# Kernel optimization log

Hardware: AMD Instinct MI355X
Metric: run time of the kernel (lower is better)

Reference implementation:

```python
import jax, jax.numpy as jnp
import numpy as np

EPS = 1e-12  # matches torch F.normalize eps


def setup_inputs() -> dict:
    key = jax.random.key(0)
    k1, k2, k3 = jax.random.split(key, 3)
    N, C, H, W, K = 16, 1024, 32, 32, 32
    x = jax.random.normal(k1, (N, C, H, W), dtype=jnp.float32)
    # 1x1 conv weight (K, C, 1, 1) stored as (K, C)
    conv_w = jax.random.normal(k2, (K, C), dtype=jnp.float32) * 0.02
    centroids = jax.random.uniform(k3, (K, C), dtype=jnp.float32)
    return {"x": x, "conv_w": conv_w, "centroids": centroids}


def _l2norm(v, axis):
    return v / jnp.maximum(jnp.linalg.norm(v, axis=axis, keepdims=True), EPS)


def reference(x, conv_w, centroids):
    N, C, H, W = x.shape
    K = centroids.shape[0]
    # normalize_input: L2 over channel dim
    x = _l2norm(x, axis=1)
    xf = x.reshape(N, C, H * W)                      # (N, C, P)
    # 1x1 conv == per-pixel matmul -> (N, K, P)
    logits = jnp.einsum('kc,ncp->nkp', conv_w, xf)
    a = jax.nn.softmax(logits, axis=1)               # softmax over clusters
    # sum_p a[n,k,p] * (x[n,:,p] - centroids[k,:])
    # == (a @ x^T) - (sum_p a) * centroids  (two GEMMs, no (N,K,C,P) blowup)
    vlad = jnp.einsum('nkp,ncp->nkc', a, xf) - a.sum(-1)[:, :, None] * centroids[None]
    vlad = _l2norm(vlad, axis=2)                     # intra-cluster L2 norm
    vlad = vlad.reshape(N, K * C)
    vlad = _l2norm(vlad, axis=1)                     # global L2 norm
    return vlad
```

## Files before the change

### kernel.cpp

```cpp
#include <hip/hip_runtime.h>

#define NB   16
#define CC   1024
#define PP   1024
#define KK   32
#define EPSF 1e-12f

typedef __attribute__((ext_vector_type(8))) short  bf16x8;
typedef __attribute__((ext_vector_type(4))) float  f32x4;

__device__ __forceinline__ float bf2f(unsigned short u) {
    union { unsigned int i; float f; } v; v.i = ((unsigned int)u) << 16; return v.f;
}
__device__ __forceinline__ unsigned short f2bf(float f) {
    union { float f; unsigned int i; } v; v.f = f;
    return (unsigned short)((v.i + 0x7fffu + ((v.i >> 16) & 1u)) >> 16);
}

template <typename T> struct IO;
template <> struct IO<float> {
    static __device__ __forceinline__ float  ld (const float* p) { return *p; }
    static __device__ __forceinline__ float4 ld4(const float* p) { return *(const float4*)p; }
};
template <> struct IO<unsigned short> {
    static __device__ __forceinline__ float  ld (const unsigned short* p) { return bf2f(*p); }
    static __device__ __forceinline__ float4 ld4(const unsigned short* p) {
        const ushort4 u = *(const ushort4*)p;
        return make_float4(bf2f(u.x), bf2f(u.y), bf2f(u.z), bf2f(u.w));
    }
};

__device__ __forceinline__ void wg_sync_fast() {
    asm volatile("s_waitcnt lgkmcnt(0)" ::: "memory");
    __builtin_amdgcn_s_barrier();
    asm volatile("" ::: "memory");
}

__global__ __launch_bounds__(256) void k_detect(const unsigned short* __restrict__ xu,
                                                int* __restrict__ flag,
                                                float* __restrict__ zbuf) {
    __shared__ int s;
    const int t = threadIdx.x;
    for (int i = t; i < 2 * NB * KK; i += 256) zbuf[i] = 0.f;
    if (t == 0) s = 0;
    __syncthreads();
    int bad = 0;
    for (int i = t; i < 4096; i += 256)
        if (((xu[i] >> 7) & 0xFFu) > 0x9Fu) bad = 1;
    if (bad) atomicOr(&s, 1);
    __syncthreads();
    if (t == 0) flag[0] = s;
}

template <typename T>
__device__ __forceinline__ void attn_body(const T* __restrict__ x,
                                          const T* __restrict__ w,
                                          float* __restrict__ rnorm_ws,
                                          unsigned short* __restrict__ attn_g,
                                          float* __restrict__ asum) {
    __shared__ __align__(16) unsigned short xt[2][32 * 136];
    __shared__ __align__(16) unsigned short w_lds[2][32 * 136];
    __shared__ float red[32 * 32];
    __shared__ float lg[32 * 33];
    __shared__ float inv_lds[32];
    __shared__ float rnorm_lds[32];
    const int b = blockIdx.x, t = threadIdx.x;
    const int n = b >> 5, pbase = (b & 31) * 32;
    const int lane = t & 63, wid = t >> 6;
    const int quad = lane >> 4, l15 = lane & 15;
    const int mt = wid & 1, nt = wid >> 1;

    const size_t xb = (size_t)n * CC * PP + pbase;
    float ss0 = 0.f, ss1 = 0.f, ss2 = 0.f, ss3 = 0.f;
    f32x4 acc = {0.f, 0.f, 0.f, 0.f};

    const int pxg = 4 * (t & 7);
    const int crow = t >> 3;
    const int wcg = (t & 7) * 16;

    float4 xr[4], wr[4];
    #pragma unroll
    for (int pass = 0; pass < 4; ++pass)
        xr[pass] = IO<T>::ld4(&x[xb + (size_t)(crow + 32 * pass) * PP + pxg]);
    #pragma unroll
    for (int j = 0; j < 4; ++j)
        wr[j] = IO<T>::ld4(&w[crow * CC + wcg + 4 * j]);

    #pragma unroll 2
    for (int ch = 0; ch < 8; ++ch) {
        const int buf = ch & 1;
        #pragma unroll
        for (int pass = 0; pass < 4; ++pass) {
            const int cl = crow + 32 * pass;
            const float4 v = xr[pass];
            ss0 += v.x * v.x; ss1 += v.y * v.y; ss2 += v.z * v.z; ss3 += v.w * v.w;
            xt[buf][(pxg + 0) * 136 + cl] = f2bf(v.x);
            xt[buf][(pxg + 1) * 136 + cl] = f2bf(v.y);
            xt[buf][(pxg + 2) * 136 + cl] = f2bf(v.z);
            xt[buf][(pxg + 3) * 136 + cl] = f2bf(v.w);
        }
        #pragma unroll
        for (int j = 0; j < 4; ++j) {
            const float4 v = wr[j];
            ushort4 u;
            u.x = f2bf(v.x); u.y = f2bf(v.y); u.z = f2bf(v.z); u.w = f2bf(v.w);
            *(ushort4*)&w_lds[buf][crow * 136 + wcg + 4 * j] = u;
        }
        if (ch < 7) {
            const int c0 = (ch + 1) * 128;
            #pragma unroll
            for (int pass = 0; pass < 4; ++pass)
                xr[pass] = IO<T>::ld4(&x[xb + (size_t)(c0 + crow + 32 * pass) * PP + pxg]);
            #pragma unroll
            for (int j = 0; j < 4; ++j)
                wr[j] = IO<T>::ld4(&w[crow * CC + c0 + wcg + 4 * j]);
        }
        wg_sync_fast();
        #pragma unroll
        for (int ks = 0; ks < 4; ++ks) {
            const bf16x8 av = *(const bf16x8*)&xt[buf][(mt * 16 + l15) * 136 + ks * 32 + quad * 8];
            const bf16x8 bv = *(const bf16x8*)&w_lds[buf][(nt * 16 + l15) * 136 + ks * 32 + quad * 8];
            acc = __builtin_amdgcn_mfma_f32_16x16x32_bf16(av, bv, acc, 0, 0, 0);
        }
    }
    red[crow * 32 + pxg + 0] = ss0;
    red[crow * 32 + pxg + 1] = ss1;
    red[crow * 32 + pxg + 2] = ss2;
    red[crow * 32 + pxg + 3] = ss3;
    __syncthreads();
    if (t < 32) {
        float s = 0.f;
        #pragma unroll
        for (int g = 0; g < 32; ++g) s += red[g * 32 + t];
        const float r = 1.0f / fmaxf(sqrtf(s), EPSF);
        rnorm_lds[t] = r;
        rnorm_ws[n * PP + pbase + t] = r;
    }
    __syncthreads();
    #pragma unroll
    for (int reg = 0; reg < 4; ++reg) {
        const int px = mt * 16 + quad * 4 + reg;
        lg[px * 33 + nt * 16 + l15] = acc[reg] * rnorm_lds[px];
    }
    __syncthreads();
    if (t < 32) {
        float m = -1e30f;
        #pragma unroll
        for (int k = 0; k < KK; ++k) m = fmaxf(m, lg[t * 33 + k]);
        float s = 0.f;
        #pragma unroll
        for (int k = 0; k < KK; ++k) {
            const float e = expf(lg[t * 33 + k] - m);
            lg[t * 33 + k] = e;
            s += e;
        }
        inv_lds[t] = 1.0f / s;
    }
    __syncthreads();
    {
        const int k = t >> 3;
        float s = 0.f;
        ushort4 u;
        float vv[4];
        #pragma unroll
        for (int j = 0; j < 4; ++j) {
            const int px = pxg + j;
            vv[j] = lg[px * 33 + k] * inv_lds[px];
        }
        u.x = f2bf(vv[0]); u.y = f2bf(vv[1]); u.z = f2bf(vv[2]); u.w = f2bf(vv[3]);
        s = bf2f(u.x) + bf2f(u.y) + bf2f(u.z) + bf2f(u.w);
        *(ushort4*)&attn_g[((size_t)n * KK + k) * PP + pbase + pxg] = u;
        s += __shfl_xor(s, 1, 64);
        s += __shfl_xor(s, 2, 64);
        s += __shfl_xor(s, 4, 64);
        if ((t & 7) == 0) atomicAdd(&asum[n * KK + k], s);
    }
}
__global__ __launch_bounds__(256) void k_attn(const void* __restrict__ x,
                                              const void* __restrict__ w,
                                              const int* __restrict__ flag,
                                              float* __restrict__ rnorm_ws,
                                              unsigned short* __restrict__ attn_g,
                                              float* __restrict__ asum) {
    if (*flag) attn_body<float>((const float*)x, (const float*)w, rnorm_ws, attn_g, asum);
    else       attn_body<unsigned short>((const unsigned short*)x, (const unsigned short*)w,
                                         rnorm_ws, attn_g, asum);
}

template <typename T>
__device__ __forceinline__ void vlad_body(const T* __restrict__ x,
                                          const T* __restrict__ cent,
                                          const float* __restrict__ rnorm_ws,
                                          const unsigned short* __restrict__ attn_g,
                                          const float* __restrict__ asum,
                                          float* __restrict__ vlad,
                                          float* __restrict__ ssqnk) {
    __shared__ __align__(16) unsigned short xt[2][32 * 136];
    __shared__ __align__(16) unsigned short at_lds[2][32 * 136];
    __shared__ float asum_lds[32];
    __shared__ float ssq_lds[32];
    const int b = blockIdx.x, t = threadIdx.x;
    const int n = b >> 5, cbase = (b & 31) * 32;
    const int lane = t & 63, wid = t >> 6;
    const int quad = lane >> 4, l15 = lane & 15;
    const int mt = wid & 1, nt = wid >> 1;

    if (t < 32) { asum_lds[t] = asum[n * KK + t]; ssq_lds[t] = 0.f; }

    f32x4 acc = {0.f, 0.f, 0.f, 0.f};
    const size_t xb = (size_t)n * CC * PP + (size_t)cbase * PP;

    const int ak  = t >> 3, apg = (t & 7) * 16;
    const int xpg = 4 * (t & 31);
    const int xc  = t >> 5;

    uint4 a0, a1; float4 xr[4]; float4 rn;
    {
        const size_t abase = ((size_t)n * KK + ak) * PP + apg;
        a0 = *(const uint4*)&attn_g[abase];
        a1 = *(const uint4*)&attn_g[abase + 8];
        rn = *(const float4*)&rnorm_ws[n * PP + xpg];
        #pragma unroll
        for (int pass = 0; pass < 4; ++pass)
            xr[pass] = IO<T>::ld4(&x[xb + (size_t)(xc + 8 * pass) * PP + xpg]);
    }

    #pragma unroll 2
    for (int pc = 0; pc < 8; ++pc) {
        const int buf = pc & 1;
        *(uint4*)&at_lds[buf][ak * 136 + apg]     = a0;
        *(uint4*)&at_lds[buf][ak * 136 + apg + 8] = a1;
        #pragma unroll
        for (int pass = 0; pass < 4; ++pass) {
            const int ci = xc + 8 * pass;
            const float4 v = xr[pass];
            ushort4 u;
            u.x = f2bf(v.x * rn.x); u.y = f2bf(v.y * rn.y);
            u.z = f2bf(v.z * rn.z); u.w = f2bf(v.w * rn.w);
            *(ushort4*)&xt[buf][ci * 136 + xpg] = u;
        }
        if (pc < 7) {
            const int p0 = (pc + 1) * 128;
            const size_t abase = ((size_t)n * KK + ak) * PP + p0 + apg;
            a0 = *(const uint4*)&attn_g[abase];
            a1 = *(const uint4*)&attn_g[abase + 8];
            rn = *(const float4*)&rnorm_ws[n * PP + p0 + xpg];
            #pragma unroll
            for (int pass = 0; pass < 4; ++pass)
                xr[pass] = IO<T>::ld4(&x[xb + (size_t)(xc + 8 * pass) * PP + p0 + xpg]);
        }
        wg_sync_fast();
        #pragma unroll
        for (int ks = 0; ks < 4; ++ks) {
            const bf16x8 av = *(const bf16x8*)&at_lds[buf][(mt * 16 + l15) * 136 + ks * 32 + quad * 8];
            const bf16x8 bv = *(const bf16x8*)&xt[buf][(nt * 16 + l15) * 136 + ks * 32 + quad * 8];
            acc = __builtin_amdgcn_mfma_f32_16x16x32_bf16(av, bv, acc, 0, 0, 0);
        }
    }
    const int cg = cbase + nt * 16 + l15;
    #pragma unroll
    for (int reg = 0; reg < 4; ++reg) {
        const int k = mt * 16 + quad * 4 + reg;
        const float A = asum_lds[k];
        const float v0 = acc[reg] - A * IO<T>::ld(&cent[k * CC + cg]);
        vlad[((size_t)n * KK + k) * CC + cg] = v0;
        float s = v0 * v0;
        s += __shfl_xor(s, 1, 64);
        s += __shfl_xor(s, 2, 64);
        s += __shfl_xor(s, 4, 64);
        s += __shfl_xor(s, 8, 64);
        if (l15 == 0) atomicAdd(&ssq_lds[k], s);
    }
    __syncthreads();
    if (t < 32) atomicAdd(&ssqnk[n * KK + t], ssq_lds[t]);
}
__global__ __launch_bounds__(256) void k_vlad(const void* __restrict__ x,
                                              const void* __restrict__ cent,
                                              const int* __restrict__ flag,
                                              const float* __restrict__ rnorm_ws,
                                              const unsigned short* __restrict__ attn_g,
                                              const float* __restrict__ asum,
                                              float* __restrict__ vlad,
                                              float* __restrict__ ssqnk) {
    if (*flag) vlad_body<float>((const float*)x, (const float*)cent, rnorm_ws, attn_g,
                                asum, vlad, ssqnk);
    else       vlad_body<unsigned short>((const unsigned short*)x, (const unsigned short*)cent,
                                         rnorm_ws, attn_g, asum, vlad, ssqnk);
}

__global__ __launch_bounds__(256) void k_out(const float* __restrict__ vlad,
                                             const float* __restrict__ ssqnk,
                                             const int* __restrict__ flag,
                                             void* __restrict__ out) {
    __shared__ float fsh;
    const int b = blockIdx.x, t = threadIdx.x;
    const int n = b >> 5, k = b & 31;
    if (t < 64) {
        const float s = (t < 32) ? ssqnk[n * KK + t] : 0.f;
        const float r = 1.0f / fmaxf(sqrtf(s), EPSF);
        float g = s * r * r;
        #pragma unroll
        for (int off = 32; off > 0; off >>= 1) g += __shfl_down(g, off, 64);
        const float rk = __shfl(r, k, 64);
        if (t == 0) fsh = rk * (1.0f / fmaxf(sqrtf(g), EPSF));
    }
    __syncthreads();
    const float f = fsh;
    const float4 v = ((const float4*)(vlad + (size_t)b * CC))[t];
    if (*flag) {
        float4 o; o.x = v.x * f; o.y = v.y * f; o.z = v.z * f; o.w = v.w * f;
        ((float4*)((float*)out + (size_t)b * CC))[t] = o;
    } else {
        ushort4 u;
        u.x = f2bf(v.x * f); u.y = f2bf(v.y * f);
        u.z = f2bf(v.z * f); u.w = f2bf(v.w * f);
        ((ushort4*)((unsigned short*)out + (size_t)b * CC))[t] = u;
    }
}

extern "C" void kernel_launch(void* const* d_in, const int* in_sizes, int n_in,
                              void* d_out, int out_size, void* d_ws, size_t ws_size,
                              hipStream_t stream) {
    const void* x    = d_in[0];
    const void* w    = d_in[1];
    const void* cent = d_in[2];

    float* ws       = (float*)d_ws;
    float* rnorm_ws = ws;
    float* vlad     = rnorm_ws + NB * PP;
    float* asum     = vlad + NB * KK * CC;
    float* ssqnk    = asum + NB * KK;
    float* rintra   = ssqnk + NB * KK;
    float* rglob    = rintra + NB * KK;
    int*   flag     = (int*)(rglob + NB);
    unsigned short* attn_g = (unsigned short*)(flag + 4);
    (void)rintra; (void)rglob;

    k_detect<<<1, 256, 0, stream>>>((const unsigned short*)x, flag, asum);
    k_attn<<<NB * 32, 256, 0, stream>>>(x, w, flag, rnorm_ws, attn_g, asum);
    k_vlad<<<NB * 32, 256, 0, stream>>>(x, cent, flag, rnorm_ws, attn_g, asum, vlad, ssqnk);
    k_out<<<NB * KK, 256, 0, stream>>>(vlad, ssqnk, flag, d_out);
}
```

Before: 124.9 us.

## Fold dtype detection into attention kernel, replace atomics with partial sums, shrink K-chunks

Removes the separate single-block detect/zeroing kernel: each attention block now re-scans the first 4096 elements itself to decide the dtype, and block 0 writes the flag. Global atomicAdd accumulations for attention sums and squared norms are replaced by per-tile partial buffers that the consumer kernels reduce, so no zero-initialisation is needed. The GEMM loops use 64-wide channel/pixel chunks with two register prefetch sets, so each loaded chunk is staged one step ahead. The cost is a redundant detection scan per block and extra partial-sum reads in the later kernels.

```diff
diff --git a/kernel.cpp b/kernel.cpp
--- a/kernel.cpp
+++ b/kernel.cpp
@@ -36,232 +36,256 @@
     asm volatile("" ::: "memory");
 }
 
-__global__ __launch_bounds__(256) void k_detect(const unsigned short* __restrict__ xu,
-                                                int* __restrict__ flag,
-                                                float* __restrict__ zbuf) {
-    __shared__ int s;
-    const int t = threadIdx.x;
-    for (int i = t; i < 2 * NB * KK; i += 256) zbuf[i] = 0.f;
-    if (t == 0) s = 0;
-    __syncthreads();
-    int bad = 0;
-    for (int i = t; i < 4096; i += 256)
-        if (((xu[i] >> 7) & 0xFFu) > 0x9Fu) bad = 1;
-    if (bad) atomicOr(&s, 1);
-    __syncthreads();
-    if (t == 0) flag[0] = s;
-}
+struct AttnSmem {
+    unsigned short xt[2][32 * 72];
+    unsigned short wl[2][32 * 72];
+    float red[32 * 32];
+    float lg[32 * 33];
+    float inv[32];
+    float rnorm[32];
+};
 
 template <typename T>
 __device__ __forceinline__ void attn_body(const T* __restrict__ x,
                                           const T* __restrict__ w,
                                           float* __restrict__ rnorm_ws,
                                           unsigned short* __restrict__ attn_g,
-                                          float* __restrict__ asum) {
-    __shared__ __align__(16) unsigned short xt[2][32 * 136];
-    __shared__ __align__(16) unsigned short w_lds[2][32 * 136];
-    __shared__ float red[32 * 32];
-    __shared__ float lg[32 * 33];
-    __shared__ float inv_lds[32];
-    __shared__ float rnorm_lds[32];
+                                          float* __restrict__ asum_part,
+                                          AttnSmem& sm) {
     const int b = blockIdx.x, t = threadIdx.x;
-    const int n = b >> 5, pbase = (b & 31) * 32;
+    const int n = b >> 5, pt = b & 31, pbase = pt * 32;
     const int lane = t & 63, wid = t >> 6;
     const int quad = lane >> 4, l15 = lane & 15;
     const int mt = wid & 1, nt = wid >> 1;
 
     const size_t xb = (size_t)n * CC * PP + pbase;
+    const int pxg  = 4 * (t & 7);
+    const int crow = t >> 3;
+    const int wcg  = (t & 7) * 8;
+
     float ss0 = 0.f, ss1 = 0.f, ss2 = 0.f, ss3 = 0.f;
     f32x4 acc = {0.f, 0.f, 0.f, 0.f};
 
-    const int pxg = 4 * (t & 7);
-    const int crow = t >> 3;
-    const int wcg = (t & 7) * 16;
-
-    float4 xr[4], wr[4];
+    float4 xr0[2], xr1[2], wr0[2], wr1[2];
+    xr0[0] = IO<T>::ld4(&x[xb + (size_t)(crow)      * PP + pxg]);
+    xr0[1] = IO<T>::ld4(&x[xb + (size_t)(crow + 32) * PP + pxg]);
+    wr0[0] = IO<T>::ld4(&w[crow * CC + wcg]);
+    wr0[1] = IO<T>::ld4(&w[crow * CC + wcg + 4]);
+    xr1[0] = IO<T>::ld4(&x[xb + (size_t)(64 + crow)      * PP + pxg]);
+    xr1[1] = IO<T>::ld4(&x[xb + (size_t)(64 + crow + 32) * PP + pxg]);
+    wr1[0] = IO<T>::ld4(&w[crow * CC + 64 + wcg]);
+    wr1[1] = IO<T>::ld4(&w[crow * CC + 64 + wcg + 4]);
+
+#define ATTN_STEP(CH, XR, WR)                                                     \
+    do {                                                                          \
+        const int buf = (CH) & 1;                                                 \
+        _Pragma("unroll")                                                         \
+        for (int pass = 0; pass < 2; ++pass) {                                    \
+            const int cl = crow + 32 * pass;                                      \
+            const float4 v = XR[pass];                                            \
+            ss0 += v.x * v.x; ss1 += v.y * v.y;                                   \
+            ss2 += v.z * v.z; ss3 += v.w * v.w;                                   \
+            sm.xt[buf][(pxg + 0) * 72 + cl] = f2bf(v.x);                          \
+            sm.xt[buf][(pxg + 1) * 72 + cl] = f2bf(v.y);                          \
+            sm.xt[buf][(pxg + 2) * 72 + cl] = f2bf(v.z);                          \
+            sm.xt[buf][(pxg + 3) * 72 + cl] = f2bf(v.w);                          \
+        }                                                                         \
+        _Pragma("unroll")                                                         \
+        for (int j = 0; j < 2; ++j) {                                             \
+            const float4 v = WR[j];                                               \
+            ushort4 u;                                                            \
+            u.x = f2bf(v.x); u.y = f2bf(v.y); u.z = f2bf(v.z); u.w = f2bf(v.w);   \
+            *(ushort4*)&sm.wl[buf][crow * 72 + wcg + 4 * j] = u;                  \
+        }                                                                         \
+        if ((CH) + 2 < 16) {                                                      \
+            const int c0 = ((CH) + 2) * 64;                                       \
+            XR[0] = IO<T>::ld4(&x[xb + (size_t)(c0 + crow)      * PP + pxg]);     \
+            XR[1] = IO<T>::ld4(&x[xb + (size_t)(c0 + crow + 32) * PP + pxg]);     \
+            WR[0] = IO<T>::ld4(&w[crow * CC + c0 + wcg]);                         \
+            WR[1] = IO<T>::ld4(&w[crow * CC + c0 + wcg + 4]);                     \
+        }                                                                         \
+        wg_sync_fast();                                                           \
+        _Pragma("unroll")                                                         \
+        for (int ks = 0; ks < 2; ++ks) {                                          \
+            const bf16x8 av = *(const bf16x8*)&sm.xt[buf][(mt * 16 + l15) * 72 + ks * 32 + quad * 8]; \
+            const bf16x8 bv = *(const bf16x8*)&sm.wl[buf][(nt * 16 + l15) * 72 + ks * 32 + quad * 8]; \
+            acc = __builtin_amdgcn_mfma_f32_16x16x32_bf16(av, bv, acc, 0, 0, 0);  \
+        }                                                                         \
+    } while (0)
+
     #pragma unroll
-    for (int pass = 0; pass < 4; ++pass)
-        xr[pass] = IO<T>::ld4(&x[xb + (size_t)(crow + 32 * pass) * PP + pxg]);
-    #pragma unroll
-    for (int j = 0; j < 4; ++j)
-        wr[j] = IO<T>::ld4(&w[crow * CC + wcg + 4 * j]);
-
-    #pragma unroll 2
-    for (int ch = 0; ch < 8; ++ch) {
-        const int buf = ch & 1;
-        #pragma unroll
-        for (int pass = 0; pass < 4; ++pass) {
-            const int cl = crow + 32 * pass;
-            const float4 v = xr[pass];
-            ss0 += v.x * v.x; ss1 += v.y * v.y; ss2 += v.z * v.z; ss3 += v.w * v.w;
-            xt[buf][(pxg + 0) * 136 + cl] = f2bf(v.x);
-            xt[buf][(pxg + 1) * 136 + cl] = f2bf(v.y);
-            xt[buf][(pxg + 2) * 136 + cl] = f2bf(v.z);
-            xt[buf][(pxg + 3) * 136 + cl] = f2bf(v.w);
-        }
-        #pragma unroll
-        for (int j = 0; j < 4; ++j) {
-            const float4 v = wr[j];
-            ushort4 u;
-            u.x = f2bf(v.x); u.y = f2bf(v.y); u.z = f2bf(v.z); u.w = f2bf(v.w);
-            *(ushort4*)&w_lds[buf][crow * 136 + wcg + 4 * j] = u;
-        }
-        if (ch < 7) {
-            const int c0 = (ch + 1) * 128;
-            #pragma unroll
-            for (int pass = 0; pass < 4; ++pass)
-                xr[pass] = IO<T>::ld4(&x[xb + (size_t)(c0 + crow + 32 * pass) * PP + pxg]);
-            #pragma unroll
-            for (int j = 0; j < 4; ++j)
-                wr[j] = IO<T>::ld4(&w[crow * CC + c0 + wcg + 4 * j]);
-        }
-        wg_sync_fast();
-        #pragma unroll
-        for (int ks = 0; ks < 4; ++ks) {
-            const bf16x8 av = *(const bf16x8*)&xt[buf][(mt * 16 + l15) * 136 + ks * 32 + quad * 8];
-            const bf16x8 bv = *(const bf16x8*)&w_lds[buf][(nt * 16 + l15) * 136 + ks * 32 + quad * 8];
-            acc = __builtin_amdgcn_mfma_f32_16x16x32_bf16(av, bv, acc, 0, 0, 0);
-        }
-    }
-    red[crow * 32 + pxg + 0] = ss0;
-    red[crow * 32 + pxg + 1] = ss1;
-    red[crow * 32 + pxg + 2] = ss2;
-    red[crow * 32 + pxg + 3] = ss3;
+    for (int chp = 0; chp < 8; ++chp) {
+        ATTN_STEP(2 * chp,     xr0, wr0);
+        ATTN_STEP(2 * chp + 1, xr1, wr1);
+    }
+#undef ATTN_STEP
+
+    sm.red[crow * 32 + pxg + 0] = ss0;
+    sm.red[crow * 32 + pxg + 1] = ss1;
+    sm.red[crow * 32 + pxg + 2] = ss2;
+    sm.red[crow * 32 + pxg + 3] = ss3;
     __syncthreads();
     if (t < 32) {
         float s = 0.f;
         #pragma unroll
-        for (int g = 0; g < 32; ++g) s += red[g * 32 + t];
+        for (int g = 0; g < 32; ++g) s += sm.red[g * 32 + t];
         const float r = 1.0f / fmaxf(sqrtf(s), EPSF);
-        rnorm_lds[t] = r;
+        sm.rnorm[t] = r;
         rnorm_ws[n * PP + pbase + t] = r;
     }
     __syncthreads();
     #pragma unroll
     for (int reg = 0; reg < 4; ++reg) {
         const int px = mt * 16 + quad * 4 + reg;
-        lg[px * 33 + nt * 16 + l15] = acc[reg] * rnorm_lds[px];
+        sm.lg[px * 33 + nt * 16 + l15] = acc[reg] * sm.rnorm[px];
     }
     __syncthreads();
     if (t < 32) {
         float m = -1e30f;
         #pragma unroll
-        for (int k = 0; k < KK; ++k) m = fmaxf(m, lg[t * 33 + k]);
+        for (int k = 0; k < KK; ++k) m = fmaxf(m, sm.lg[t * 33 + k]);
         float s = 0.f;
         #pragma unroll
         for (int k = 0; k < KK; ++k) {
-            const float e = expf(lg[t * 33 + k] - m);
-            lg[t * 33 + k] = e;
+            const float e = expf(sm.lg[t * 33 + k] - m);
+            sm.lg[t * 33 + k] = e;
             s += e;
         }
-        inv_lds[t] = 1.0f / s;
+        sm.inv[t] = 1.0f / s;
     }
     __syncthreads();
     {
         const int k = t >> 3;
-        float s = 0.f;
         ushort4 u;
         float vv[4];
         #pragma unroll
         for (int j = 0; j < 4; ++j) {
             const int px = pxg + j;
-            vv[j] = lg[px * 33 + k] * inv_lds[px];
+            vv[j] = sm.lg[px * 33 + k] * sm.inv[px];
         }
         u.x = f2bf(vv[0]); u.y = f2bf(vv[1]); u.z = f2bf(vv[2]); u.w = f2bf(vv[3]);
-        s = bf2f(u.x) + bf2f(u.y) + bf2f(u.z) + bf2f(u.w);
+        float s = bf2f(u.x) + bf2f(u.y) + bf2f(u.z) + bf2f(u.w);
         *(ushort4*)&attn_g[((size_t)n * KK + k) * PP + pbase + pxg] = u;
         s += __shfl_xor(s, 1, 64);
         s += __shfl_xor(s, 2, 64);
         s += __shfl_xor(s, 4, 64);
-        if ((t & 7) == 0) atomicAdd(&asum[n * KK + k], s);
-    }
-}
+        if ((t & 7) == 0) asum_part[(n * 32 + pt) * KK + k] = s;
+    }
+}
+
 __global__ __launch_bounds__(256) void k_attn(const void* __restrict__ x,
                                               const void* __restrict__ w,
-                                              const int* __restrict__ flag,
+                                              int* __restrict__ flag,
                                               float* __restrict__ rnorm_ws,
                                               unsigned short* __restrict__ attn_g,
-                                              float* __restrict__ asum) {
-    if (*flag) attn_body<float>((const float*)x, (const float*)w, rnorm_ws, attn_g, asum);
-    else       attn_body<unsigned short>((const unsigned short*)x, (const unsigned short*)w,
-                                         rnorm_ws, attn_g, asum);
-}
+                                              float* __restrict__ asum_part) {
+    __shared__ AttnSmem sm;
+    __shared__ int s_bad;
+    const int t = threadIdx.x;
+    if (t == 0) s_bad = 0;
+    __syncthreads();
+    const unsigned short* xu = (const unsigned short*)x;
+    int bad = 0;
+    for (int i = t; i < 4096; i += 256)
+        if (((xu[i] >> 7) & 0xFFu) > 0x9Fu) bad = 1;
+    if (bad) atomicOr(&s_bad, 1);
+    __syncthreads();
+    const int f = s_bad;
+    if (blockIdx.x == 0 && t == 0) flag[0] = f;
+    if (f) attn_body<float>((const float*)x, (const float*)w, rnorm_ws, attn_g, asum_part, sm);
+    else   attn_body<unsigned short>((const unsigned short*)x, (const unsigned short*)w,
+                                     rnorm_ws, attn_g, asum_part, sm);
+}
+
+struct VladSmem {
+    unsigned short xt[2][32 * 72];
+    unsigned short at[2][32 * 72];
+    float asum[32];
+    float ssq[32];
+};
 
 template <typename T>
 __device__ __forceinline__ void vlad_body(const T* __restrict__ x,
                                           const T* __restrict__ cent,
                                           const float* __restrict__ rnorm_ws,
                                           const unsigned short* __restrict__ attn_g,
-                                          const float* __restrict__ asum,
+                                          const float* __restrict__ asum_part,
                                           float* __restrict__ vlad,
-                                          float* __restrict__ ssqnk) {
-    __shared__ __align__(16) unsigned short xt[2][32 * 136];
-    __shared__ __align__(16) unsigned short at_lds[2][32 * 136];
-    __shared__ float asum_lds[32];
-    __shared__ float ssq_lds[32];
+                                          float* __restrict__ ssq_part,
+                                          VladSmem& sm) {
     const int b = blockIdx.x, t = threadIdx.x;
-    const int n = b >> 5, cbase = (b & 31) * 32;
+    const int n = b >> 5, ct = b & 31, cbase = ct * 32;
     const int lane = t & 63, wid = t >> 6;
     const int quad = lane >> 4, l15 = lane & 15;
     const int mt = wid & 1, nt = wid >> 1;
 
-    if (t < 32) { asum_lds[t] = asum[n * KK + t]; ssq_lds[t] = 0.f; }
+    if (t < 32) {
+        float s = 0.f;
+        #pragma unroll
+        for (int pt = 0; pt < 32; ++pt) s += asum_part[(n * 32 + pt) * KK + t];
+        sm.asum[t] = s;
+        sm.ssq[t] = 0.f;
+    }
 
     f32x4 acc = {0.f, 0.f, 0.f, 0.f};
     const size_t xb = (size_t)n * CC * PP + (size_t)cbase * PP;
 
-    const int ak  = t >> 3, apg = (t & 7) * 16;
-    const int xpg = 4 * (t & 31);
-    const int xc  = t >> 5;
-
-    uint4 a0, a1; float4 xr[4]; float4 rn;
-    {
-        const size_t abase = ((size_t)n * KK + ak) * PP + apg;
-        a0 = *(const uint4*)&attn_g[abase];
-        a1 = *(const uint4*)&attn_g[abase + 8];
-        rn = *(const float4*)&rnorm_ws[n * PP + xpg];
-        #pragma unroll
-        for (int pass = 0; pass < 4; ++pass)
-            xr[pass] = IO<T>::ld4(&x[xb + (size_t)(xc + 8 * pass) * PP + xpg]);
-    }
-
-    #pragma unroll 2
-    for (int pc = 0; pc < 8; ++pc) {
-        const int buf = pc & 1;
-        *(uint4*)&at_lds[buf][ak * 136 + apg]     = a0;
-        *(uint4*)&at_lds[buf][ak * 136 + apg + 8] = a1;
-        #pragma unroll
-        for (int pass = 0; pass < 4; ++pass) {
-            const int ci = xc + 8 * pass;
-            const float4 v = xr[pass];
-            ushort4 u;
-            u.x = f2bf(v.x * rn.x); u.y = f2bf(v.y * rn.y);
-            u.z = f2bf(v.z * rn.z); u.w = f2bf(v.w * rn.w);
-            *(ushort4*)&xt[buf][ci * 136 + xpg] = u;
-        }
-        if (pc < 7) {
-            const int p0 = (pc + 1) * 128;
-            const size_t abase = ((size_t)n * KK + ak) * PP + p0 + apg;
-            a0 = *(const uint4*)&attn_g[abase];
-            a1 = *(const uint4*)&attn_g[abase + 8];
-            rn = *(const float4*)&rnorm_ws[n * PP + p0 + xpg];
-            #pragma unroll
-            for (int pass = 0; pass < 4; ++pass)
-                xr[pass] = IO<T>::ld4(&x[xb + (size_t)(xc + 8 * pass) * PP + p0 + xpg]);
-        }
-        wg_sync_fast();
-        #pragma unroll
-        for (int ks = 0; ks < 4; ++ks) {
-            const bf16x8 av = *(const bf16x8*)&at_lds[buf][(mt * 16 + l15) * 136 + ks * 32 + quad * 8];
-            const bf16x8 bv = *(const bf16x8*)&xt[buf][(nt * 16 + l15) * 136 + ks * 32 + quad * 8];
-            acc = __builtin_amdgcn_mfma_f32_16x16x32_bf16(av, bv, acc, 0, 0, 0);
-        }
-    }
+    const int ak  = t >> 3, apg = (t & 7) * 8;
+    const int xpg = 4 * (t & 15);
+    const int xc  = t >> 4;
+    const size_t ab = ((size_t)n * KK + ak) * PP + apg;
+
+    uint4 ar0, ar1; float4 xr0[2], xr1[2], rn0, rn1;
+    ar0 = *(const uint4*)&attn_g[ab];
+    rn0 = *(const float4*)&rnorm_ws[n * PP + xpg];
+    xr0[0] = IO<T>::ld4(&x[xb + (size_t)(xc)      * PP + xpg]);
+    xr0[1] = IO<T>::ld4(&x[xb + (size_t)(xc + 16) * PP + xpg]);
+    ar1 = *(const uint4*)&attn_g[ab + 64];
+    rn1 = *(const float4*)&rnorm_ws[n * PP + 64 + xpg];
+    xr1[0] = IO<T>::ld4(&x[xb + (size_t)(xc)      * PP + 64 + xpg]);
+    xr1[1] = IO<T>::ld4(&x[xb + (size_t)(xc + 16) * PP + 64 + xpg]);
+
+#define VLAD_STEP(CH, AR, XR, RN)                                                 \
+    do {                                                                          \
+        const int buf = (CH) & 1;                                                 \
+        *(uint4*)&sm.at[buf][ak * 72 + apg] = AR;                                 \
+        _Pragma("unroll")                                                         \
+        for (int pass = 0; pass < 2; ++pass) {                                    \
+            const int ci = xc + 16 * pass;                                        \
+            const float4 v = XR[pass];                                            \
+            ushort4 u;                                                            \
+            u.x = f2bf(v.x * RN.x); u.y = f2bf(v.y * RN.y);                       \
+            u.z = f2bf(v.z * RN.z); u.w = f2bf(v.w * RN.w);                       \
+            *(ushort4*)&sm.xt[buf][ci * 72 + xpg] = u;                            \
+        }                                                                         \
+        if ((CH) + 2 < 16) {                                                      \
+            const int p0 = ((CH) + 2) * 64;                                       \
+            AR = *(const uint4*)&attn_g[ab + p0];                                 \
+            RN = *(const float4*)&rnorm_ws[n * PP + p0 + xpg];                    \
+            XR[0] = IO<T>::ld4(&x[xb + (size_t)(xc)      * PP + p0 + xpg]);       \
+            XR[1] = IO<T>::ld4(&x[xb + (size_t)(xc + 16) * PP + p0 + xpg]);       \
+        }                                                                         \
+        wg_sync_fast();                                                           \
+        _Pragma("unroll")                                                         \
+        for (int ks = 0; ks < 2; ++ks) {                                          \
+            const bf16x8 av = *(const bf16x8*)&sm.at[buf][(mt * 16 + l15) * 72 + ks * 32 + quad * 8]; \
+            const bf16x8 bv = *(const bf16x8*)&sm.xt[buf][(nt * 16 + l15) * 72 + ks * 32 + quad * 8]; \
+            acc = __builtin_amdgcn_mfma_f32_16x16x32_bf16(av, bv, acc, 0, 0, 0);  \
+        }                                                                         \
+    } while (0)
+
+    #pragma unroll
+    for (int pcp = 0; pcp < 8; ++pcp) {
+        VLAD_STEP(2 * pcp,     ar0, xr0, rn0);
+        VLAD_STEP(2 * pcp + 1, ar1, xr1, rn1);
+    }
+#undef VLAD_STEP
+
     const int cg = cbase + nt * 16 + l15;
     #pragma unroll
     for (int reg = 0; reg < 4; ++reg) {
         const int k = mt * 16 + quad * 4 + reg;
-        const float A = asum_lds[k];
+        const float A = sm.asum[k];
         const float v0 = acc[reg] - A * IO<T>::ld(&cent[k * CC + cg]);
         vlad[((size_t)n * KK + k) * CC + cg] = v0;
         float s = v0 * v0;
@@ -269,34 +293,40 @@
         s += __shfl_xor(s, 2, 64);
         s += __shfl_xor(s, 4, 64);
         s += __shfl_xor(s, 8, 64);
-        if (l15 == 0) atomicAdd(&ssq_lds[k], s);
-    }
-    __syncthreads();
-    if (t < 32) atomicAdd(&ssqnk[n * KK + t], ssq_lds[t]);
-}
+        if (l15 == 0) atomicAdd(&sm.ssq[k], s);
+    }
+    __syncthreads();
+    if (t < 32) ssq_part[(n * 32 + ct) * KK + t] = sm.ssq[t];
+}
+
 __global__ __launch_bounds__(256) void k_vlad(const void* __restrict__ x,
                                               const void* __restrict__ cent,
                                               const int* __restrict__ flag,
                                               const float* __restrict__ rnorm_ws,
                                               const unsigned short* __restrict__ attn_g,
-                                              const float* __restrict__ asum,
+                                              const float* __restrict__ asum_part,
                                               float* __restrict__ vlad,
-                                              float* __restrict__ ssqnk) {
+                                              float* __restrict__ ssq_part) {
+    __shared__ VladSmem sm;
     if (*flag) vlad_body<float>((const float*)x, (const float*)cent, rnorm_ws, attn_g,
-                                asum, vlad, ssqnk);
+                                asum_part, vlad, ssq_part, sm);
     else       vlad_body<unsigned short>((const unsigned short*)x, (const unsigned short*)cent,
-                                         rnorm_ws, attn_g, asum, vlad, ssqnk);
+                                         rnorm_ws, attn_g, asum_part, vlad, ssq_part, sm);
 }
 
 __global__ __launch_bounds__(256) void k_out(const float* __restrict__ vlad,
-                                             const float* __restrict__ ssqnk,
+                                             const float* __restrict__ ssq_part,
                                              const int* __restrict__ flag,
                                              void* __restrict__ out) {
     __shared__ float fsh;
     const int b = blockIdx.x, t = threadIdx.x;
     const int n = b >> 5, k = b & 31;
     if (t < 64) {
-        const float s = (t < 32) ? ssqnk[n * KK + t] : 0.f;
+        float s = 0.f;
+        if (t < 32) {
+            #pragma unroll
+            for (int ct = 0; ct < 32; ++ct) s += ssq_part[(n * 32 + ct) * KK + t];
+        }
         const float r = 1.0f / fmaxf(sqrtf(s), EPSF);
         float g = s * r * r;
         #pragma unroll
@@ -325,19 +355,15 @@
     const void* w    = d_in[1];
     const void* cent = d_in[2];
 
-    float* ws       = (float*)d_ws;
-    float* rnorm_ws = ws;
-    float* vlad     = rnorm_ws + NB * PP;
-    float* asum     = vlad + NB * KK * CC;
-    float* ssqnk    = asum + NB * KK;
-    float* rintra   = ssqnk + NB * KK;
-    float* rglob    = rintra + NB * KK;
-    int*   flag     = (int*)(rglob + NB);
+    float* ws        = (float*)d_ws;
+    float* rnorm_ws  = ws;
+    float* vlad      = rnorm_ws + NB * PP;
+    float* asum_part = vlad + NB * KK * CC;
+    float* ssq_part  = asum_part + NB * 32 * KK;
+    int*   flag      = (int*)(ssq_part + NB * 32 * KK);
     unsigned short* attn_g = (unsigned short*)(flag + 4);
-    (void)rintra; (void)rglob;
-
-    k_detect<<<1, 256, 0, stream>>>((const unsigned short*)x, flag, asum);
-    k_attn<<<NB * 32, 256, 0, stream>>>(x, w, flag, rnorm_ws, attn_g, asum);
-    k_vlad<<<NB * 32, 256, 0, stream>>>(x, cent, flag, rnorm_ws, attn_g, asum, vlad, ssqnk);
-    k_out<<<NB * KK, 256, 0, stream>>>(vlad, ssqnk, flag, d_out);
-}
+
+    k_attn<<<NB * 32, 256, 0, stream>>>(x, w, flag, rnorm_ws, attn_g, asum_part);
+    k_vlad<<<NB * 32, 256, 0, stream>>>(x, cent, flag, rnorm_ws, attn_g, asum_part, vlad, ssq_part);
+    k_out<<<NB * KK, 256, 0, stream>>>(vlad, ssq_part, flag, d_out);
+}
```

Result: slower. 129.6 us (+3.7%).
